# Performance work log

Measured on AMD Instinct MI355X. Metric: run time of the kernel, lower is better.

Reference implementation:

```python
import jax, jax.numpy as jnp
import numpy as np

B, S, K = 128, 196, 512   # batch, encoder seq, keys_hidden_size
T_CAP = 16                # caption length (out_seq_len = 15)
V, E, H = 32000, 512, 512 # vocab, embedding, hidden


def setup_inputs() -> dict:
    key = jax.random.key(0)
    ks = jax.random.split(key, 16)
    sc = lambda fan_in: 1.0 / np.sqrt(fan_in)
    return {
        "features": jax.random.normal(ks[0], (B, S, K), jnp.float32),
        "captions": jax.random.randint(ks[1], (B, T_CAP), 0, V),
        "emb": jax.random.normal(ks[2], (V, E), jnp.float32) * 0.02,
        "fc1_w": jax.random.normal(ks[3], (H, E), jnp.float32) * sc(E),
        "fc1_b": jnp.zeros((H,), jnp.float32),
        "att_wq": jax.random.normal(ks[4], (H, H), jnp.float32) * sc(H),
        "att_wk": jax.random.normal(ks[5], (H, K), jnp.float32) * sc(K),
        "att_v": jax.random.normal(ks[6], (H,), jnp.float32) * sc(H),
        "fc0_w": jax.random.normal(ks[7], (H, K), jnp.float32) * sc(K),
        "fc0_b": jnp.zeros((H,), jnp.float32),
        "gru_wih": jax.random.normal(ks[8], (3 * H, 2 * H), jnp.float32) * sc(2 * H),
        "gru_whh": jax.random.normal(ks[9], (3 * H, H), jnp.float32) * sc(H),
        "gru_bih": jnp.zeros((3 * H,), jnp.float32),
        "gru_bhh": jnp.zeros((3 * H,), jnp.float32),
        "fc2_w": jax.random.normal(ks[10], (V, H), jnp.float32) * sc(H),
        "fc2_b": jnp.zeros((V,), jnp.float32),
    }


def reference(features, captions, emb, fc1_w, fc1_b, att_wq, att_wk, att_v,
              fc0_w, fc0_b, gru_wih, gru_whh, gru_bih, gru_bhh, fc2_w, fc2_b):
    # embed captions and project: (B, T_CAP, H)
    x = emb[captions] @ fc1_w.T + fc1_b
    # precompute key projection for Bahdanau attention: (B, S, H)
    keys_proj = features @ att_wk.T

    def step(h, x_t):
        # Bahdanau additive attention
        q = h @ att_wq.T                                   # (B, H)
        scores = jnp.tanh(q[:, None, :] + keys_proj) @ att_v  # (B, S)
        w = jax.nn.softmax(scores, axis=1)
        context = jnp.einsum('bs,bsk->bk', w, features)    # (B, K)
        context = context @ fc0_w.T + fc0_b                # fc_0 -> (B, H)
        rnn_in = jnp.concatenate([x_t, context], axis=-1)  # (B, 2H)
        # GRU cell, torch gate order (r, z, n)
        gi = rnn_in @ gru_wih.T + gru_bih
        gh = h @ gru_whh.T + gru_bhh
        ir, iz, inn = jnp.split(gi, 3, axis=-1)
        hr, hz, hn = jnp.split(gh, 3, axis=-1)
        r = jax.nn.sigmoid(ir + hr)
        z = jax.nn.sigmoid(iz + hz)
        n = jnp.tanh(inn + r * hn)
        h_new = (1.0 - z) * n + z * h
        out = h_new @ fc2_w.T + fc2_b                      # fc_2 -> (B, V)
        return h_new, out

    out_seq_len = captions.shape[1] - 1
    xs = jnp.swapaxes(x[:, :out_seq_len], 0, 1)            # (T, B, H)
    h0 = jnp.zeros((features.shape[0], fc0_b.shape[0]), features.dtype)
    _, outs = jax.lax.scan(step, h0, xs)                   # (T, B, V)
    return jnp.swapaxes(outs, 0, 1)                        # (B, T, V)
```

## Files before the change

kernel.cpp:

```cpp
#include <hip/hip_runtime.h>

typedef _Float16 half_t;
typedef float    floatx4 __attribute__((ext_vector_type(4)));
typedef _Float16 halfx8  __attribute__((ext_vector_type(8)));
typedef _Float16 halfx2  __attribute__((ext_vector_type(2)));

__device__ __forceinline__ float tanh_f(float x) {
  float e = __expf(2.0f * x);
  return 1.0f - 2.0f / (e + 1.0f);
}
__device__ __forceinline__ float sigmoid_f(float x) {
  return 1.0f / (1.0f + __expf(-x));
}

__device__ __forceinline__ void gl16(const void* g, void* s) {
  __builtin_amdgcn_global_load_lds((__attribute__((address_space(1))) unsigned int*)g,
                                   (__attribute__((address_space(3))) unsigned int*)s,
                                   16, 0, 0);
}

__device__ __forceinline__ int xcd_swz(int bid, int nwg) {
  int q = nwg >> 3, r = nwg & 7, x = bid & 7, p = bid >> 3;
  return (x < r ? x * (q + 1) : r * (q + 1) + (x - r) * q) + p;
}

__device__ __forceinline__ void gbar(int* cnt, int* gen, int nb) {
  __syncthreads();
  if (threadIdx.x == 0) {
    int g = __hip_atomic_load(gen, __ATOMIC_RELAXED, __HIP_MEMORY_SCOPE_AGENT);
    if (__hip_atomic_fetch_add(cnt, 1, __ATOMIC_ACQ_REL, __HIP_MEMORY_SCOPE_AGENT) == nb - 1) {
      __hip_atomic_store(cnt, 0, __ATOMIC_RELAXED, __HIP_MEMORY_SCOPE_AGENT);
      __hip_atomic_store(gen, g + 1, __ATOMIC_RELEASE, __HIP_MEMORY_SCOPE_AGENT);
    } else {
      while (__hip_atomic_load(gen, __ATOMIC_ACQUIRE, __HIP_MEMORY_SCOPE_AGENT) == g) {
        __builtin_amdgcn_s_sleep(8);
      }
    }
  }
  __syncthreads();
}

__device__ __forceinline__ void cvt4(const float* __restrict__ src,
                                     half_t* __restrict__ dst, int blk) {
  int i = (blk * 256 + threadIdx.x) * 4;
  float4 v = *(const float4*)(src + i);
  halfx2 a; a[0] = (half_t)v.x; a[1] = (half_t)v.y;
  halfx2 b; b[0] = (half_t)v.z; b[1] = (half_t)v.w;
  *(halfx2*)(dst + i) = a;
  *(halfx2*)(dst + i + 2) = b;
}

__global__ __launch_bounds__(256) void k_prep(const float* __restrict__ fc2_w, half_t* __restrict__ fc2w_h,
                                              const float* __restrict__ features, half_t* __restrict__ featf,
                                              const float* __restrict__ fc1_w, half_t* __restrict__ fc1w_h,
                                              const float* __restrict__ att_wk, const float* __restrict__ fc0_w,
                                              half_t* __restrict__ wkfc0,
                                              const float* __restrict__ gru_whh, const float* __restrict__ att_wq,
                                              half_t* __restrict__ bcat2,
                                              const float* __restrict__ gru_wih, half_t* __restrict__ wihx,
                                              half_t* __restrict__ wihc,
                                              const float* __restrict__ emb, const int* __restrict__ cap,
                                              half_t* __restrict__ embg,
                                              const float* __restrict__ fc0_b, float* __restrict__ biasc,
                                              float4* __restrict__ zbase) {
  const int bb = blockIdx.x, tid = threadIdx.x;
  if (bb < 16000) {
    cvt4(fc2_w, fc2w_h, bb);
  } else if (bb < 28544) {
    cvt4(features, featf, bb - 16000);
  } else if (bb < 28800) {
    cvt4(fc1_w, fc1w_h, bb - 28544);
  } else if (bb < 29056) {
    cvt4(att_wk, wkfc0, bb - 28800);
  } else if (bb < 29312) {
    cvt4(fc0_w, wkfc0 + (size_t)512 * 512, bb - 29056);
  } else if (bb < 30080) {
    cvt4(gru_whh, bcat2, bb - 29312);
  } else if (bb < 30336) {
    cvt4(att_wq, bcat2 + (size_t)1536 * 512, bb - 30080);
  } else if (bb < 31872) {
    int row = bb - 30336, j = tid * 2;
    float2 a = *(const float2*)(gru_wih + (size_t)row * 1024 + j);
    float2 b = *(const float2*)(gru_wih + (size_t)row * 1024 + 512 + j);
    halfx2 ax; ax[0] = (half_t)a.x; ax[1] = (half_t)a.y;
    halfx2 bx; bx[0] = (half_t)b.x; bx[1] = (half_t)b.y;
    *(halfx2*)(wihx + (size_t)row * 512 + j) = ax;
    *(halfx2*)(wihc + (size_t)row * 512 + j) = bx;
  } else if (bb < 33792) {
    int row = bb - 31872;
    int b = row / 15, t = row - b * 15;
    int c = cap[b * 16 + t];
    const float* s = emb + (size_t)c * 512;
    int e = tid * 2;
    float2 v = *(const float2*)(s + e);
    halfx2 o; o[0] = (half_t)v.x; o[1] = (half_t)v.y;
    *(halfx2*)(embg + (size_t)row * 512 + e) = o;
  } else if (bb < 33796) {
    int i = (bb - 33792) * 256 + tid;
    biasc[i] = (i < 512) ? 0.f : fc0_b[i - 512];
  } else {
    zbase[(size_t)(bb - 33796) * 256 + tid] = make_float4(0.f, 0.f, 0.f, 0.f);
  }
}

template <bool OUT_F16>
__device__ __forceinline__ void gemm128_body(const half_t* __restrict__ Ap,
                                             const half_t* __restrict__ Bp,
                                             const float* __restrict__ bias,
                                             void* __restrict__ Cp,
                                             const int Kd, const int ldc,
                                             const int m0, const int n0,
                                             char* smem) {
  constexpr int ABYTES = 128 * 32 * 2;
  constexpr int BBYTES = 128 * 32 * 2;

  const int l = threadIdx.x & 63;
  const int w = threadIdx.x >> 6;

  const half_t* gA = Ap + (size_t)(m0 + w * 32 + (l >> 2)) * Kd + (l & 3) * 8;
  const half_t* gB = Bp + (size_t)(n0 + w * 32 + (l >> 2)) * Kd + (l & 3) * 8;

  const int fr = l & 15;
  const int kq = (l >> 4) * 8;
  const int mh = (w & 1) * 64;
  const int nh = (w >> 1) * 64;

  floatx4 acc[4][4];
#pragma unroll
  for (int i = 0; i < 4; ++i)
#pragma unroll
    for (int j = 0; j < 4; ++j) { floatx4 z = {0.f, 0.f, 0.f, 0.f}; acc[i][j] = z; }

  const int NT = Kd >> 5;

  auto stage = [&](int tt) {
    const int k0 = tt * 32;
    char* aD = smem + (tt & 1) * ABYTES;
    char* bD = smem + 2 * ABYTES + (tt & 1) * BBYTES;
    const half_t* g = gA + k0;
    gl16(g, aD + (w * 32) * 64);
    gl16(g + (size_t)16 * Kd, aD + (w * 32 + 16) * 64);
    const half_t* g2 = gB + k0;
    gl16(g2, bD + (w * 32) * 64);
    gl16(g2 + (size_t)16 * Kd, bD + (w * 32 + 16) * 64);
  };

  stage(0);

  for (int t = 0; t < NT; ++t) {
    __syncthreads();
    if (t + 1 < NT) stage(t + 1);
    const char* aB = smem + (t & 1) * ABYTES;
    const char* bB = smem + 2 * ABYTES + (t & 1) * BBYTES;
    halfx8 af[4], bf[4];
#pragma unroll
    for (int i = 0; i < 4; ++i) {
      af[i] = *(const halfx8*)((const half_t*)aB + (size_t)(mh + i * 16 + fr) * 32 + kq);
      bf[i] = *(const halfx8*)((const half_t*)bB + (size_t)(nh + i * 16 + fr) * 32 + kq);
    }
#pragma unroll
    for (int i = 0; i < 4; ++i)
#pragma unroll
      for (int j = 0; j < 4; ++j)
        acc[i][j] = __builtin_amdgcn_mfma_f32_16x16x32_f16(af[i], bf[j], acc[i][j], 0, 0, 0);
  }

#pragma unroll
  for (int j = 0; j < 4; ++j) {
    const int n = n0 + nh + j * 16 + fr;
    const float bv = bias ? bias[n] : 0.0f;
#pragma unroll
    for (int i = 0; i < 4; ++i) {
      const int mb = m0 + mh + i * 16 + (l >> 4) * 4;
#pragma unroll
      for (int r = 0; r < 4; ++r) {
        const float v = acc[i][j][r] + bv;
        const size_t ci = (size_t)(mb + r) * ldc + n;
        if constexpr (OUT_F16) ((half_t*)Cp)[ci] = (half_t)v;
        else                   ((float*)Cp)[ci] = v;
      }
    }
  }
}

template <bool OUT_F16>
__global__ __launch_bounds__(256) void k_gemm_lds(const half_t* __restrict__ Ap,
                                                  const half_t* __restrict__ Bp,
                                                  const float* __restrict__ bias,
                                                  void* __restrict__ Cp,
                                                  int Kd, int ldc) {
  __shared__ __align__(16) char smem[32768];
  gemm128_body<OUT_F16>(Ap, Bp, bias, Cp, Kd, ldc,
                        blockIdx.y * 128, blockIdx.x * 128, smem);
}

__global__ __launch_bounds__(256) void k_kpfp(const half_t* __restrict__ featf,
                                              const half_t* __restrict__ wkfc0,
                                              const float* __restrict__ biasc,
                                              half_t* __restrict__ kpfp) {
  __shared__ __align__(16) char smem[32768];
  const int w = (blockIdx.x & 7) * 196 + (blockIdx.x >> 3);
  const int n0 = (w & 7) * 128;
  const int m0 = (w >> 3) * 128;
  gemm128_body<true>(featf, wkfc0, biasc, kpfp, 512, 1024, m0, n0, smem);
}

__global__ __launch_bounds__(256) void k_fc2_final(const half_t* __restrict__ hall,
                                                   const half_t* __restrict__ fc2w,
                                                   const float* __restrict__ fc2b,
                                                   float* __restrict__ outp) {
  __shared__ __align__(16) char smem[32768];
  const int w = xcd_swz(blockIdx.x, 3750);
  const int m0 = (w % 15) * 128;
  const int n0 = (w / 15) * 128;
  gemm128_body<false>(hall, fc2w, fc2b, outp, 512, 32000, m0, n0, smem);
}

__global__ __launch_bounds__(256) void k_scores(const half_t* __restrict__ kpfp,
                                                const float* __restrict__ ghq,
                                                const float* __restrict__ attv,
                                                float* __restrict__ scores) {
  int w = blockIdx.x * 4 + (threadIdx.x >> 6);
  int l = threadIdx.x & 63;
  int b = w / 196;
  halfx8 kv = *(const halfx8*)(kpfp + (size_t)w * 1024 + l * 8);
  const float* qr = ghq + (size_t)b * 2048 + 1536 + l * 8;
  float4 q0 = *(const float4*)qr;
  float4 q1 = *(const float4*)(qr + 4);
  float4 a0 = *(const float4*)(attv + l * 8);
  float4 a1 = *(const float4*)(attv + l * 8 + 4);
  float acc = a0.x * tanh_f(q0.x + (float)kv[0]);
  acc += a0.y * tanh_f(q0.y + (float)kv[1]);
  acc += a0.z * tanh_f(q0.z + (float)kv[2]);
  acc += a0.w * tanh_f(q0.w + (float)kv[3]);
  acc += a1.x * tanh_f(q1.x + (float)kv[4]);
  acc += a1.y * tanh_f(q1.y + (float)kv[5]);
  acc += a1.z * tanh_f(q1.z + (float)kv[6]);
  acc += a1.w * tanh_f(q1.w + (float)kv[7]);
#pragma unroll
  for (int off = 32; off > 0; off >>= 1) acc += __shfl_xor(acc, off, 64);
  if (l == 0) scores[w] = acc;
}

__global__ __launch_bounds__(256) void k_ctx(const float* __restrict__ scores,
                                             const half_t* __restrict__ kpfp,
                                             half_t* __restrict__ ctxo) {
  const int b = blockIdx.x, kt = blockIdx.y * 128, t = threadIdx.x;
  __shared__ float sw[196], red[256];
  float sc = (t < 196) ? scores[b * 196 + t] : -1e30f;
  red[t] = sc; __syncthreads();
  for (int o = 128; o > 0; o >>= 1) { if (t < o) red[t] = fmaxf(red[t], red[t + o]); __syncthreads(); }
  float mx = red[0]; __syncthreads();
  float e = (t < 196) ? __expf(sc - mx) : 0.f;
  red[t] = e; __syncthreads();
  for (int o = 128; o > 0; o >>= 1) { if (t < o) red[t] += red[t + o]; __syncthreads(); }
  float inv = 1.0f / red[0];
  if (t < 196) sw[t] = e * inv;
  __syncthreads();
  const int kk = t & 127, half = t >> 7, s0 = half * 98;
  const half_t* fp = kpfp + (size_t)(b * 196 + s0) * 1024 + 512 + kt + kk;
  float acc = 0.f;
#pragma unroll 7
  for (int i = 0; i < 98; ++i) acc += sw[s0 + i] * (float)fp[(size_t)i * 1024];
  red[t] = acc; __syncthreads();
  if (t < 128) ctxo[(size_t)b * 512 + kt + t] = (half_t)(red[t] + red[t + 128]);
}

__global__ __launch_bounds__(256, 1) void k_cell(const half_t* __restrict__ ctxo,
                                                 const half_t* __restrict__ wihc,
                                                 float* __restrict__ gic,
                                                 const float* __restrict__ gix,
                                                 const float* __restrict__ bih,
                                                 const float* __restrict__ bhh,
                                                 float* __restrict__ ghq,
                                                 float* __restrict__ hbuf,
                                                 half_t* __restrict__ h_h,
                                                 half_t* __restrict__ hall,
                                                 const half_t* __restrict__ bcat2,
                                                 int* __restrict__ bar, int step) {
  __shared__ __align__(16) char smem[32768];
  const int blk = blockIdx.x, tid = threadIdx.x;
  const int nb = gridDim.x;

  if (blk < 12)
    gemm128_body<false>(ctxo, wihc, nullptr, gic, 512, 1536, 0, blk * 128, smem);
  gbar(bar, bar + 1, nb);

  for (int it = blk * 256 + tid; it < 32768; it += nb * 256) {
    const int b = it >> 8, n = (it & 255) * 2;
    const float* gx = gix + (size_t)(b * 15 + step) * 1536;
    const float* gc = gic + (size_t)b * 1536;
    const float* gh = ghq + (size_t)b * 2048;
    float2 hv = *(float2*)(hbuf + (size_t)b * 512 + n);
    float2 res;
#pragma unroll
    for (int u = 0; u < 2; ++u) {
      const int nn = n + u;
      float ir  = gx[nn]        + gc[nn]        + bih[nn];
      float iz  = gx[nn + 512]  + gc[nn + 512]  + bih[nn + 512];
      float in_ = gx[nn + 1024] + gc[nn + 1024] + bih[nn + 1024];
      float hr  = gh[nn]        + bhh[nn];
      float hz  = gh[nn + 512]  + bhh[nn + 512];
      float hn  = gh[nn + 1024] + bhh[nn + 1024];
      float r = sigmoid_f(ir + hr);
      float z = sigmoid_f(iz + hz);
      float g2 = tanh_f(in_ + r * hn);
      float hnew = (1.0f - z) * g2 + z * (u ? hv.y : hv.x);
      if (u) res.y = hnew; else res.x = hnew;
    }
    *(float2*)(hbuf + (size_t)b * 512 + n) = res;
    halfx2 h2; h2[0] = (half_t)res.x; h2[1] = (half_t)res.y;
    *(halfx2*)(h_h + (size_t)b * 512 + n) = h2;
    *(halfx2*)(hall + (size_t)(b * 15 + step) * 512 + n) = h2;
  }
  gbar(bar, bar + 1, nb);

  if (blk < 16)
    gemm128_body<false>(h_h, bcat2, nullptr, ghq, 512, 2048, 0, blk * 128, smem);
}

extern "C" void kernel_launch(void* const* d_in, const int* in_sizes, int n_in,
                              void* d_out, int out_size, void* d_ws, size_t ws_size,
                              hipStream_t stream) {
  (void)in_sizes; (void)n_in; (void)out_size; (void)ws_size;
  const float* features = (const float*)d_in[0];
  const int*   captions = (const int*)d_in[1];
  const float* emb      = (const float*)d_in[2];
  const float* fc1_w    = (const float*)d_in[3];
  const float* fc1_b    = (const float*)d_in[4];
  const float* att_wq   = (const float*)d_in[5];
  const float* att_wk   = (const float*)d_in[6];
  const float* att_v    = (const float*)d_in[7];
  const float* fc0_w    = (const float*)d_in[8];
  const float* fc0_b    = (const float*)d_in[9];
  const float* gru_wih  = (const float*)d_in[10];
  const float* gru_whh  = (const float*)d_in[11];
  const float* gru_bih  = (const float*)d_in[12];
  const float* gru_bhh  = (const float*)d_in[13];
  const float* fc2_w    = (const float*)d_in[14];
  const float* fc2_b    = (const float*)d_in[15];
  float* out = (float*)d_out;

  char* p = (char*)d_ws;
  half_t* kpfp   = (half_t*)p; p += (size_t)25088 * 1024 * 2;
  half_t* fc2w_h = (half_t*)p; p += (size_t)32000 * 512 * 2;
  float*  gix    = (float*)p;  p += (size_t)1920 * 1536 * 4;
  half_t* wihx_h = (half_t*)p; p += (size_t)1536 * 512 * 2;
  half_t* wihc_h = (half_t*)p; p += (size_t)1536 * 512 * 2;
  half_t* bcat2  = (half_t*)p; p += (size_t)2048 * 512 * 2;
  half_t* wkfc0  = (half_t*)p; p += (size_t)1024 * 512 * 2;
  half_t* fc1w_h = (half_t*)p; p += (size_t)512 * 512 * 2;
  half_t* embg_h = (half_t*)p; p += (size_t)1920 * 512 * 2;
  half_t* xproj_h= (half_t*)p; p += (size_t)1920 * 512 * 2;
  float*  biasc  = (float*)p;  p += (size_t)1024 * 4;
  float*  ghq    = (float*)p;  p += (size_t)128 * 2048 * 4;
  float*  hbuf   = (float*)p;  p += (size_t)128 * 512 * 4;
  int*    bar    = (int*)p;    p += 16;
  float*  scores = (float*)p;  p += (size_t)128 * 196 * 4;
  float*  gic    = (float*)p;  p += (size_t)128 * 1536 * 4;
  half_t* ctxo   = (half_t*)p; p += (size_t)128 * 512 * 2;
  half_t* h_h    = (half_t*)p; p += (size_t)128 * 512 * 2;
  half_t* featf  = (half_t*)p; p += (size_t)25088 * 512 * 2;
  half_t* hall   = (half_t*)p; p += (size_t)1920 * 512 * 2;

  k_prep<<<dim3(34117), 256, 0, stream>>>(fc2_w, fc2w_h, features, featf,
                                          fc1_w, fc1w_h, att_wk, fc0_w, wkfc0,
                                          gru_whh, att_wq, bcat2,
                                          gru_wih, wihx_h, wihc_h,
                                          emb, captions, embg_h,
                                          fc0_b, biasc, (float4*)ghq);
  k_gemm_lds<true><<<dim3(4, 15), 256, 0, stream>>>(embg_h, fc1w_h, fc1_b, xproj_h, 512, 512);
  k_kpfp<<<dim3(1568), 256, 0, stream>>>(featf, wkfc0, biasc, kpfp);
  k_gemm_lds<false><<<dim3(12, 15), 256, 0, stream>>>(xproj_h, wihx_h, nullptr, gix, 512, 1536);

  for (int t = 0; t < 15; ++t) {
    k_scores<<<dim3(6272), 256, 0, stream>>>(kpfp, ghq, att_v, scores);
    k_ctx<<<dim3(128, 4), 256, 0, stream>>>(scores, kpfp, ctxo);
    k_cell<<<dim3(28), 256, 0, stream>>>(ctxo, wihc_h, gic, gix, gru_bih, gru_bhh,
                                         ghq, hbuf, h_h, hall, bcat2, bar, t);
  }
  k_fc2_final<<<dim3(3750), 256, 0, stream>>>(hall, fc2w_h, fc2_b, out);
}
```

Before: 1.333 ms.

## Replace grid-barrier cell kernel with separate launches and stage fc2 output via LDS

The persistent k_cell kernel, which used software grid barriers across 28 blocks, is split into three ordinary launches per step: a context-input GEMM, an elementwise gates kernel and a hidden-state GEMM. This removes the atomic spin barriers but adds two extra kernel launches per timestep. Separately, the final fc2 GEMM now stages accumulators through shared memory in two halves so the fp32 output is written as coalesced float4 rows with the bias added, instead of scattered scalar stores.

Measured after the change: 1.201 ms. -9.9%, faster.

```diff
diff --git a/kernel.cpp b/kernel.cpp
--- a/kernel.cpp
+++ b/kernel.cpp
@@ -22,22 +22,6 @@
 __device__ __forceinline__ int xcd_swz(int bid, int nwg) {
   int q = nwg >> 3, r = nwg & 7, x = bid & 7, p = bid >> 3;
   return (x < r ? x * (q + 1) : r * (q + 1) + (x - r) * q) + p;
-}
-
-__device__ __forceinline__ void gbar(int* cnt, int* gen, int nb) {
-  __syncthreads();
-  if (threadIdx.x == 0) {
-    int g = __hip_atomic_load(gen, __ATOMIC_RELAXED, __HIP_MEMORY_SCOPE_AGENT);
-    if (__hip_atomic_fetch_add(cnt, 1, __ATOMIC_ACQ_REL, __HIP_MEMORY_SCOPE_AGENT) == nb - 1) {
-      __hip_atomic_store(cnt, 0, __ATOMIC_RELAXED, __HIP_MEMORY_SCOPE_AGENT);
-      __hip_atomic_store(gen, g + 1, __ATOMIC_RELEASE, __HIP_MEMORY_SCOPE_AGENT);
-    } else {
-      while (__hip_atomic_load(gen, __ATOMIC_ACQUIRE, __HIP_MEMORY_SCOPE_AGENT) == g) {
-        __builtin_amdgcn_s_sleep(8);
-      }
-    }
-  }
-  __syncthreads();
 }
 
 __device__ __forceinline__ void cvt4(const float* __restrict__ src,
@@ -103,14 +87,11 @@
   }
 }
 
-template <bool OUT_F16>
-__device__ __forceinline__ void gemm128_body(const half_t* __restrict__ Ap,
+__device__ __forceinline__ void gemm128_mfma(const half_t* __restrict__ Ap,
                                              const half_t* __restrict__ Bp,
-                                             const float* __restrict__ bias,
-                                             void* __restrict__ Cp,
-                                             const int Kd, const int ldc,
+                                             const int Kd,
                                              const int m0, const int n0,
-                                             char* smem) {
+                                             char* smem, floatx4 (&acc)[4][4]) {
   constexpr int ABYTES = 128 * 32 * 2;
   constexpr int BBYTES = 128 * 32 * 2;
 
@@ -125,7 +106,6 @@
   const int mh = (w & 1) * 64;
   const int nh = (w >> 1) * 64;
 
-  floatx4 acc[4][4];
 #pragma unroll
   for (int i = 0; i < 4; ++i)
 #pragma unroll
@@ -164,10 +144,26 @@
       for (int j = 0; j < 4; ++j)
         acc[i][j] = __builtin_amdgcn_mfma_f32_16x16x32_f16(af[i], bf[j], acc[i][j], 0, 0, 0);
   }
+}
+
+template <bool OUT_F16>
+__device__ __forceinline__ void gemm128_body(const half_t* __restrict__ Ap,
+                                             const half_t* __restrict__ Bp,
+                                             const float* __restrict__ bias,
+                                             void* __restrict__ Cp,
+                                             const int Kd, const int ldc,
+                                             const int m0, const int n0,
+                                             char* smem) {
+  const int l = threadIdx.x & 63;
+  const int w = threadIdx.x >> 6;
+  const int mh = (w & 1) * 64;
+  const int nh = (w >> 1) * 64;
+  floatx4 acc[4][4];
+  gemm128_mfma(Ap, Bp, Kd, m0, n0, smem, acc);
 
 #pragma unroll
   for (int j = 0; j < 4; ++j) {
-    const int n = n0 + nh + j * 16 + fr;
+    const int n = n0 + nh + j * 16 + (l & 15);
     const float bv = bias ? bias[n] : 0.0f;
 #pragma unroll
     for (int i = 0; i < 4; ++i) {
@@ -209,11 +205,43 @@
                                                    const half_t* __restrict__ fc2w,
                                                    const float* __restrict__ fc2b,
                                                    float* __restrict__ outp) {
-  __shared__ __align__(16) char smem[32768];
-  const int w = xcd_swz(blockIdx.x, 3750);
-  const int m0 = (w % 15) * 128;
-  const int n0 = (w / 15) * 128;
-  gemm128_body<false>(hall, fc2w, fc2b, outp, 512, 32000, m0, n0, smem);
+  __shared__ __align__(16) char smem[64 * 132 * 4];
+  const int wk = xcd_swz(blockIdx.x, 3750);
+  const int m0 = (wk % 15) * 128;
+  const int n0 = (wk / 15) * 128;
+
+  const int tid = threadIdx.x;
+  const int l = tid & 63;
+  const int w = tid >> 6;
+  const int nh = (w >> 1) * 64;
+
+  floatx4 acc[4][4];
+  gemm128_mfma(hall, fc2w, 512, m0, n0, smem, acc);
+
+  const float4 bv4 = *(const float4*)(fc2b + n0 + (tid & 31) * 4);
+  float* sf = (float*)smem;
+
+#pragma unroll
+  for (int h = 0; h < 2; ++h) {
+    __syncthreads();
+    if ((w & 1) == h) {
+#pragma unroll
+      for (int i = 0; i < 4; ++i)
+#pragma unroll
+        for (int j = 0; j < 4; ++j)
+#pragma unroll
+          for (int r = 0; r < 4; ++r)
+            sf[(i * 16 + (l >> 4) * 4 + r) * 132 + nh + j * 16 + (l & 15)] = acc[i][j][r];
+    }
+    __syncthreads();
+#pragma unroll
+    for (int it = 0; it < 8; ++it) {
+      const int row = it * 8 + (tid >> 5);
+      float4 v = *(const float4*)&sf[row * 132 + (tid & 31) * 4];
+      v.x += bv4.x; v.y += bv4.y; v.z += bv4.z; v.w += bv4.w;
+      *(float4*)(outp + (size_t)(m0 + h * 64 + row) * 32000 + n0 + (tid & 31) * 4) = v;
+    }
+  }
 }
 
 __global__ __launch_bounds__(256) void k_scores(const half_t* __restrict__ kpfp,
@@ -266,57 +294,33 @@
   if (t < 128) ctxo[(size_t)b * 512 + kt + t] = (half_t)(red[t] + red[t + 128]);
 }
 
-__global__ __launch_bounds__(256, 1) void k_cell(const half_t* __restrict__ ctxo,
-                                                 const half_t* __restrict__ wihc,
-                                                 float* __restrict__ gic,
-                                                 const float* __restrict__ gix,
-                                                 const float* __restrict__ bih,
-                                                 const float* __restrict__ bhh,
-                                                 float* __restrict__ ghq,
-                                                 float* __restrict__ hbuf,
-                                                 half_t* __restrict__ h_h,
-                                                 half_t* __restrict__ hall,
-                                                 const half_t* __restrict__ bcat2,
-                                                 int* __restrict__ bar, int step) {
-  __shared__ __align__(16) char smem[32768];
-  const int blk = blockIdx.x, tid = threadIdx.x;
-  const int nb = gridDim.x;
-
-  if (blk < 12)
-    gemm128_body<false>(ctxo, wihc, nullptr, gic, 512, 1536, 0, blk * 128, smem);
-  gbar(bar, bar + 1, nb);
-
-  for (int it = blk * 256 + tid; it < 32768; it += nb * 256) {
-    const int b = it >> 8, n = (it & 255) * 2;
-    const float* gx = gix + (size_t)(b * 15 + step) * 1536;
-    const float* gc = gic + (size_t)b * 1536;
-    const float* gh = ghq + (size_t)b * 2048;
-    float2 hv = *(float2*)(hbuf + (size_t)b * 512 + n);
-    float2 res;
-#pragma unroll
-    for (int u = 0; u < 2; ++u) {
-      const int nn = n + u;
-      float ir  = gx[nn]        + gc[nn]        + bih[nn];
-      float iz  = gx[nn + 512]  + gc[nn + 512]  + bih[nn + 512];
-      float in_ = gx[nn + 1024] + gc[nn + 1024] + bih[nn + 1024];
-      float hr  = gh[nn]        + bhh[nn];
-      float hz  = gh[nn + 512]  + bhh[nn + 512];
-      float hn  = gh[nn + 1024] + bhh[nn + 1024];
-      float r = sigmoid_f(ir + hr);
-      float z = sigmoid_f(iz + hz);
-      float g2 = tanh_f(in_ + r * hn);
-      float hnew = (1.0f - z) * g2 + z * (u ? hv.y : hv.x);
-      if (u) res.y = hnew; else res.x = hnew;
-    }
-    *(float2*)(hbuf + (size_t)b * 512 + n) = res;
-    halfx2 h2; h2[0] = (half_t)res.x; h2[1] = (half_t)res.y;
-    *(halfx2*)(h_h + (size_t)b * 512 + n) = h2;
-    *(halfx2*)(hall + (size_t)(b * 15 + step) * 512 + n) = h2;
-  }
-  gbar(bar, bar + 1, nb);
-
-  if (blk < 16)
-    gemm128_body<false>(h_h, bcat2, nullptr, ghq, 512, 2048, 0, blk * 128, smem);
+__global__ __launch_bounds__(256) void k_gates(const float* __restrict__ gix,
+                                               const float* __restrict__ gic,
+                                               const float* __restrict__ ghq,
+                                               const float* __restrict__ bih,
+                                               const float* __restrict__ bhh,
+                                               float* __restrict__ hbuf,
+                                               half_t* __restrict__ hh,
+                                               half_t* __restrict__ hall, int step) {
+  int idx = blockIdx.x * 256 + threadIdx.x;
+  int b = idx >> 9, n = idx & 511;
+  const float* gx = gix + (size_t)(b * 15 + step) * 1536;
+  const float* gc = gic + (size_t)b * 1536;
+  const float* gh = ghq + (size_t)b * 2048;
+  float ir  = gx[n]        + gc[n]        + bih[n];
+  float iz  = gx[n + 512]  + gc[n + 512]  + bih[n + 512];
+  float in_ = gx[n + 1024] + gc[n + 1024] + bih[n + 1024];
+  float hr  = gh[n]        + bhh[n];
+  float hz  = gh[n + 512]  + bhh[n + 512];
+  float hn  = gh[n + 1024] + bhh[n + 1024];
+  float r = sigmoid_f(ir + hr);
+  float z = sigmoid_f(iz + hz);
+  float nn = tanh_f(in_ + r * hn);
+  float hv = (1.0f - z) * nn + z * hbuf[idx];
+  hbuf[idx] = hv;
+  half_t h16 = (half_t)hv;
+  hh[idx] = h16;
+  hall[(size_t)(b * 15 + step) * 512 + n] = h16;
 }
 
 extern "C" void kernel_launch(void* const* d_in, const int* in_sizes, int n_in,
@@ -362,6 +366,7 @@
   half_t* h_h    = (half_t*)p; p += (size_t)128 * 512 * 2;
   half_t* featf  = (half_t*)p; p += (size_t)25088 * 512 * 2;
   half_t* hall   = (half_t*)p; p += (size_t)1920 * 512 * 2;
+  (void)bar;
 
   k_prep<<<dim3(34117), 256, 0, stream>>>(fc2_w, fc2w_h, features, featf,
                                           fc1_w, fc1w_h, att_wk, fc0_w, wkfc0,
@@ -376,8 +381,9 @@
   for (int t = 0; t < 15; ++t) {
     k_scores<<<dim3(6272), 256, 0, stream>>>(kpfp, ghq, att_v, scores);
     k_ctx<<<dim3(128, 4), 256, 0, stream>>>(scores, kpfp, ctxo);
-    k_cell<<<dim3(28), 256, 0, stream>>>(ctxo, wihc_h, gic, gix, gru_bih, gru_bhh,
-                                         ghq, hbuf, h_h, hall, bcat2, bar, t);
+    k_gemm_lds<false><<<dim3(12, 1), 256, 0, stream>>>(ctxo, wihc_h, nullptr, gic, 512, 1536);
+    k_gates<<<dim3(256), 256, 0, stream>>>(gix, gic, ghq, gru_bih, gru_bhh, hbuf, h_h, hall, t);
+    k_gemm_lds<false><<<dim3(16, 1), 256, 0, stream>>>(h_h, bcat2, nullptr, ghq, 512, 2048);
   }
   k_fc2_final<<<dim3(3750), 256, 0, stream>>>(hall, fc2w_h, fc2_b, out);
 }
```
